# Performance work log

Hardware: AMD Instinct MI355X
Metric: run time of the kernel (lower is better)

The kernel has to match this reference:

```python
import jax, jax.numpy as jnp
import numpy as np

D_MODEL = 1024
NUM_HEADS = 16
D_K = D_MODEL // NUM_HEADS


def setup_inputs() -> dict:
    key = jax.random.key(0)
    ks = jax.random.split(key, 11)
    B, S = 2, 2048
    scale = 1.0 / np.sqrt(D_MODEL)
    inp = {
        "v": jax.random.normal(ks[0], (B, S, D_MODEL), jnp.float32),
        "k": jax.random.normal(ks[1], (B, S, D_MODEL), jnp.float32),
        "q": jax.random.normal(ks[2], (B, S, D_MODEL), jnp.float32),
        "Wv": jax.random.normal(ks[3], (D_MODEL, D_MODEL), jnp.float32) * scale,
        "bv": jax.random.normal(ks[4], (D_MODEL,), jnp.float32) * 0.01,
        "Wk": jax.random.normal(ks[5], (D_MODEL, D_MODEL), jnp.float32) * scale,
        "bk": jax.random.normal(ks[6], (D_MODEL,), jnp.float32) * 0.01,
        "Wq": jax.random.normal(ks[7], (D_MODEL, D_MODEL), jnp.float32) * scale,
        "bq": jax.random.normal(ks[8], (D_MODEL,), jnp.float32) * 0.01,
        "Wo": jax.random.normal(ks[9], (D_MODEL, D_MODEL), jnp.float32) * scale,
        "bo": jax.random.normal(ks[10], (D_MODEL,), jnp.float32) * 0.01,
    }
    return inp


def reference(v, k, q, Wv, bv, Wk, bk, Wq, bq, Wo, bo):
    B, S, _ = q.shape
    # Linear projections (torch Linear: x @ W.T + b)
    vp = v @ Wv.T + bv
    kp = k @ Wk.T + bk
    qp = q @ Wq.T + bq
    # Split heads: [B, S, H, Dk]
    vp = vp.reshape(B, S, NUM_HEADS, D_K)
    kp = kp.reshape(B, S, NUM_HEADS, D_K)
    qp = qp.reshape(B, S, NUM_HEADS, D_K)
    # Scores [B, H, S, S], scaled softmax attention
    scores = jnp.einsum("bqhd,bkhd->bhqk", qp, kp) / jnp.sqrt(jnp.float32(D_K)).astype(qp.dtype)
    attn = jax.nn.softmax(scores, axis=-1)
    out = jnp.einsum("bhqk,bkhd->bqhd", attn, vp)
    out = out.reshape(B, S, D_MODEL)
    return out @ Wo.T + bo
```

## Files before the change

kernel.cpp:

```cpp
#include <hip/hip_runtime.h>
#include <math.h>

#define D 1024
#define NH 16
#define DK 64
#define S_LEN 2048
#define QSCALE 0.18033688011112f

using short8 = __attribute__((ext_vector_type(8))) short;
using f32x4  = __attribute__((ext_vector_type(4))) float;

#define MFMA16(a, b, c) __builtin_amdgcn_mfma_f32_16x16x32_bf16((a), (b), (c), 0, 0, 0)
#define EXP2F(x) __builtin_amdgcn_exp2f(x)

__device__ inline unsigned short f2bf(float f) {
    union { float f; unsigned u; } v; v.f = f;
    unsigned r = v.u + 0x7fffu + ((v.u >> 16) & 1u);
    return (unsigned short)(r >> 16);
}

__device__ inline void gload16(const unsigned short* g, unsigned short* l) {
    __builtin_amdgcn_global_load_lds(
        (const __attribute__((address_space(1))) void*)g,
        (__attribute__((address_space(3))) void*)l, 16, 0, 0);
}

struct CvtP {
    const float* s[7];
    unsigned short* d[7];
};
__global__ __launch_bounds__(256) void cvt_all(CvtP p, int inpBlocks, int wBlocks) {
    int bx = blockIdx.x;
    int seg, boff;
    if (bx < 3 * inpBlocks) { seg = bx / inpBlocks; boff = bx - seg * inpBlocks; }
    else { int t = bx - 3 * inpBlocks; seg = 3 + t / wBlocks; boff = t - (seg - 3) * wBlocks; }
    int i = (boff * 256 + threadIdx.x) * 4;
    float4 f = *(const float4*)(p.s[seg] + i);
    ushort4 u;
    u.x = f2bf(f.x); u.y = f2bf(f.y); u.z = f2bf(f.z); u.w = f2bf(f.w);
    *(ushort4*)(p.d[seg] + i) = u;
}

__global__ __launch_bounds__(256) void gemm_qkv(
    const unsigned short* __restrict__ qb, const unsigned short* __restrict__ kb,
    const unsigned short* __restrict__ vb,
    const unsigned short* __restrict__ Wqb, const unsigned short* __restrict__ Wkb,
    const unsigned short* __restrict__ Wvb,
    const float* __restrict__ bq, const float* __restrict__ bk, const float* __restrict__ bv,
    unsigned short* __restrict__ Qp, unsigned short* __restrict__ Kp,
    unsigned short* __restrict__ Vt)
{
    __shared__ unsigned short sA[128 * 32];
    __shared__ unsigned short sB[64 * 32];

    const int z = blockIdx.z;
    const unsigned short* X = (z == 0) ? qb : (z == 1) ? kb : vb;
    const unsigned short* W = (z == 0) ? Wqb : (z == 1) ? Wkb : Wvb;
    const float* bias = (z == 0) ? bq : (z == 1) ? bk : bv;

    const int tid = threadIdx.x, lane = tid & 63, w = tid >> 6;
    const int wy = w & 1, wx = w >> 1, r = lane & 15, q = lane >> 4;
    const int m0 = blockIdx.x * 128, n0 = blockIdx.y * 64;
    const int lrow = tid >> 2, lkc = (tid & 3) * 8;

    const unsigned short* Xg = X + (size_t)(m0 + lrow) * D + lkc;
    const unsigned short* Wg = W + (size_t)(n0 + lrow) * D + lkc;

    f32x4 acc[4][2];
    #pragma unroll
    for (int mi = 0; mi < 4; ++mi)
        #pragma unroll
        for (int ni = 0; ni < 2; ++ni) acc[mi][ni] = (f32x4){0.f, 0.f, 0.f, 0.f};

    for (int k0 = 0; k0 < D; k0 += 32) {
        __syncthreads();
        gload16(Xg + k0,          sA + w * 512);
        gload16(Xg + 64 * D + k0, sA + 2048 + w * 512);
        gload16(Wg + k0,          sB + w * 512);
        __syncthreads();
        short8 af[4], bfr[2];
        #pragma unroll
        for (int mi = 0; mi < 4; ++mi)
            af[mi] = *(const short8*)(sA + (wy * 64 + mi * 16 + r) * 32 + q * 8);
        #pragma unroll
        for (int ni = 0; ni < 2; ++ni)
            bfr[ni] = *(const short8*)(sB + (wx * 32 + ni * 16 + r) * 32 + q * 8);
        #pragma unroll
        for (int mi = 0; mi < 4; ++mi)
            #pragma unroll
            for (int ni = 0; ni < 2; ++ni)
                acc[mi][ni] = MFMA16(af[mi], bfr[ni], acc[mi][ni]);
    }

    float bcol[2];
    #pragma unroll
    for (int ni = 0; ni < 2; ++ni) bcol[ni] = bias[n0 + wx * 32 + ni * 16 + r];

    #pragma unroll
    for (int mi = 0; mi < 4; ++mi)
        #pragma unroll
        for (int ni = 0; ni < 2; ++ni)
            #pragma unroll
            for (int reg = 0; reg < 4; ++reg) {
                int row = m0 + wy * 64 + mi * 16 + q * 4 + reg;
                int col = n0 + wx * 32 + ni * 16 + r;
                float val = acc[mi][ni][reg] + bcol[ni];
                if (z == 0) {
                    Qp[(size_t)row * D + col] = f2bf(val * QSCALE);
                } else if (z == 1) {
                    Kp[(size_t)row * D + col] = f2bf(val);
                } else {
                    int bb = row >> 11, s = row & (S_LEN - 1);
                    int h = col >> 6, dk = col & 63;
                    Vt[(((size_t)bb * NH + h) * DK + dk) * (size_t)S_LEN + s] = f2bf(val);
                }
            }
}

__global__ __launch_bounds__(256) void gemm_o(
    const unsigned short* __restrict__ X, const unsigned short* __restrict__ W,
    const float* __restrict__ bias, float* __restrict__ out)
{
    __shared__ unsigned short sA[128 * 32];
    __shared__ unsigned short sB[64 * 32];

    const int tid = threadIdx.x, lane = tid & 63, w = tid >> 6;
    const int wy = w & 1, wx = w >> 1, r = lane & 15, q = lane >> 4;
    const int m0 = blockIdx.x * 128, n0 = blockIdx.y * 64;
    const int lrow = tid >> 2, lkc = (tid & 3) * 8;

    const unsigned short* Xg = X + (size_t)(m0 + lrow) * D + lkc;
    const unsigned short* Wg = W + (size_t)(n0 + lrow) * D + lkc;

    f32x4 acc[4][2];
    #pragma unroll
    for (int mi = 0; mi < 4; ++mi)
        #pragma unroll
        for (int ni = 0; ni < 2; ++ni) acc[mi][ni] = (f32x4){0.f, 0.f, 0.f, 0.f};

    for (int k0 = 0; k0 < D; k0 += 32) {
        __syncthreads();
        gload16(Xg + k0,          sA + w * 512);
        gload16(Xg + 64 * D + k0, sA + 2048 + w * 512);
        gload16(Wg + k0,          sB + w * 512);
        __syncthreads();
        short8 af[4], bfr[2];
        #pragma unroll
        for (int mi = 0; mi < 4; ++mi)
            af[mi] = *(const short8*)(sA + (wy * 64 + mi * 16 + r) * 32 + q * 8);
        #pragma unroll
        for (int ni = 0; ni < 2; ++ni)
            bfr[ni] = *(const short8*)(sB + (wx * 32 + ni * 16 + r) * 32 + q * 8);
        #pragma unroll
        for (int mi = 0; mi < 4; ++mi)
            #pragma unroll
            for (int ni = 0; ni < 2; ++ni)
                acc[mi][ni] = MFMA16(af[mi], bfr[ni], acc[mi][ni]);
    }

    float bcol[2];
    #pragma unroll
    for (int ni = 0; ni < 2; ++ni) bcol[ni] = bias[n0 + wx * 32 + ni * 16 + r];

    #pragma unroll
    for (int mi = 0; mi < 4; ++mi)
        #pragma unroll
        for (int ni = 0; ni < 2; ++ni)
            #pragma unroll
            for (int reg = 0; reg < 4; ++reg) {
                int row = m0 + wy * 64 + mi * 16 + q * 4 + reg;
                int col = n0 + wx * 32 + ni * 16 + r;
                out[(size_t)row * D + col] = acc[mi][ni][reg] + bcol[ni];
            }
}

__global__ __launch_bounds__(256) void attn_bf16(
    const unsigned short* __restrict__ Qp, const unsigned short* __restrict__ Kp,
    const unsigned short* __restrict__ Vt, unsigned short* __restrict__ AO)
{
    __shared__ unsigned short sK[2 * 2048];
    __shared__ unsigned short sV[2 * 2048];
    __shared__ unsigned short sP[4][32][72];

    const int tid = threadIdx.x, lane = tid & 63, w = tid >> 6;
    const int r = lane & 15, q = lane >> 4;
    const int q0 = blockIdx.x * 128;
    const int h = blockIdx.y, b = blockIdx.z;
    const int S = S_LEN;

    const unsigned short* Qbase = Qp + ((size_t)b * S + q0 + 32 * w) * D + h * DK;
    short8 qf[2][2];
    #pragma unroll
    for (int rb = 0; rb < 2; ++rb)
        #pragma unroll
        for (int c = 0; c < 2; ++c)
            qf[rb][c] = *(const short8*)(Qbase + (size_t)(rb * 16 + r) * D + c * 32 + q * 8);

    const int srow = tid >> 2, scol = (tid & 3) * 8;
    const unsigned short* Kg = Kp + ((size_t)b * S + srow) * D + h * DK + scol;
    const unsigned short* Vg = Vt + (((size_t)b * NH + h) * DK + srow) * (size_t)S + scol;

    f32x4 O[2][4];
    float psum[2][4];
    #pragma unroll
    for (int rb = 0; rb < 2; ++rb)
        #pragma unroll
        for (int i = 0; i < 4; ++i) { O[rb][i] = (f32x4){0.f, 0.f, 0.f, 0.f}; psum[rb][i] = 0.f; }

    for (int kv0 = 0; kv0 < S; kv0 += 64) {
        __syncthreads();
        gload16(Kg + (size_t)kv0 * D,      sK + w * 512);
        gload16(Kg + (size_t)kv0 * D + 32, sK + 2048 + w * 512);
        gload16(Vg + kv0,                  sV + w * 512);
        gload16(Vg + kv0 + 32,             sV + 2048 + w * 512);
        __syncthreads();

        f32x4 sc[2][4];
        #pragma unroll
        for (int j = 0; j < 4; ++j) {
            short8 kf0 = *(const short8*)(sK + (16 * j + r) * 32 + q * 8);
            short8 kf1 = *(const short8*)(sK + 2048 + (16 * j + r) * 32 + q * 8);
            #pragma unroll
            for (int rb = 0; rb < 2; ++rb) {
                f32x4 t = (f32x4){0.f, 0.f, 0.f, 0.f};
                t = MFMA16(qf[rb][0], kf0, t);
                t = MFMA16(qf[rb][1], kf1, t);
                sc[rb][j] = t;
            }
        }

        #pragma unroll
        for (int rb = 0; rb < 2; ++rb)
            #pragma unroll
            for (int reg = 0; reg < 4; ++reg) {
                float p0 = EXP2F(fminf(sc[rb][0][reg], 30.f));
                float p1 = EXP2F(fminf(sc[rb][1][reg], 30.f));
                float p2 = EXP2F(fminf(sc[rb][2][reg], 30.f));
                float p3 = EXP2F(fminf(sc[rb][3][reg], 30.f));
                psum[rb][reg] += (p0 + p1) + (p2 + p3);
                int row = rb * 16 + q * 4 + reg;
                sP[w][row][r]      = f2bf(p0);
                sP[w][row][16 + r] = f2bf(p1);
                sP[w][row][32 + r] = f2bf(p2);
                sP[w][row][48 + r] = f2bf(p3);
            }

        short8 pf[2][2];
        #pragma unroll
        for (int rb = 0; rb < 2; ++rb) {
            pf[rb][0] = *(const short8*)(&sP[w][rb * 16 + r][q * 8]);
            pf[rb][1] = *(const short8*)(&sP[w][rb * 16 + r][32 + q * 8]);
        }

        #pragma unroll
        for (int nb = 0; nb < 4; ++nb) {
            short8 vf0 = *(const short8*)(sV + (16 * nb + r) * 32 + q * 8);
            short8 vf1 = *(const short8*)(sV + 2048 + (16 * nb + r) * 32 + q * 8);
            #pragma unroll
            for (int rb = 0; rb < 2; ++rb) {
                O[rb][nb] = MFMA16(pf[rb][0], vf0, O[rb][nb]);
                O[rb][nb] = MFMA16(pf[rb][1], vf1, O[rb][nb]);
            }
        }
    }

    float inv[2][4];
    #pragma unroll
    for (int rb = 0; rb < 2; ++rb)
        #pragma unroll
        for (int reg = 0; reg < 4; ++reg) {
            float l = psum[rb][reg];
            #pragma unroll
            for (int off = 8; off > 0; off >>= 1) l += __shfl_xor(l, off);
            inv[rb][reg] = 1.0f / l;
        }

    unsigned short* Ob = AO + ((size_t)b * S + q0 + 32 * w) * D + h * DK;
    #pragma unroll
    for (int rb = 0; rb < 2; ++rb)
        #pragma unroll
        for (int reg = 0; reg < 4; ++reg)
            #pragma unroll
            for (int nb = 0; nb < 4; ++nb)
                Ob[(size_t)(rb * 16 + q * 4 + reg) * D + nb * 16 + r] =
                    f2bf(O[rb][nb][reg] * inv[rb][reg]);
}

extern "C" void kernel_launch(void* const* d_in, const int* in_sizes, int n_in,
                              void* d_out, int out_size, void* d_ws, size_t ws_size,
                              hipStream_t stream)
{
    const float* v  = (const float*)d_in[0];
    const float* k  = (const float*)d_in[1];
    const float* q  = (const float*)d_in[2];
    const float* Wv = (const float*)d_in[3];
    const float* bv = (const float*)d_in[4];
    const float* Wk = (const float*)d_in[5];
    const float* bk = (const float*)d_in[6];
    const float* Wq = (const float*)d_in[7];
    const float* bq = (const float*)d_in[8];
    const float* Wo = (const float*)d_in[9];
    const float* bo = (const float*)d_in[10];
    float* out = (float*)d_out;

    const int BS = in_sizes[0] / D;
    const int S  = S_LEN;
    const int B  = BS / S;

    char* ws = (char*)d_ws;
    unsigned short* qb  = (unsigned short*)(ws);
    unsigned short* kb  = (unsigned short*)(ws + 8388608);
    unsigned short* vb  = (unsigned short*)(ws + 16777216);
    unsigned short* Wqb = (unsigned short*)(ws + 25165824);
    unsigned short* Wkb = (unsigned short*)(ws + 27262976);
    unsigned short* Wvb = (unsigned short*)(ws + 29360128);
    unsigned short* Wob = (unsigned short*)(ws + 31457280);
    unsigned short* Qp  = (unsigned short*)(ws + 33554432);
    unsigned short* Kp  = (unsigned short*)(ws + 41943040);
    unsigned short* Vt  = (unsigned short*)(ws + 50331648);
    unsigned short* AO  = qb;

    dim3 blk(256);
    const int nInp = BS * D, nW = D * D;
    const int inpBlocks = nInp / 1024, wBlocks = nW / 1024;

    CvtP cp;
    cp.s[0] = q;  cp.d[0] = qb;
    cp.s[1] = k;  cp.d[1] = kb;
    cp.s[2] = v;  cp.d[2] = vb;
    cp.s[3] = Wq; cp.d[3] = Wqb;
    cp.s[4] = Wk; cp.d[4] = Wkb;
    cp.s[5] = Wv; cp.d[5] = Wvb;
    cp.s[6] = Wo; cp.d[6] = Wob;
    cvt_all<<<3 * inpBlocks + 4 * wBlocks, blk, 0, stream>>>(cp, inpBlocks, wBlocks);

    dim3 qkvgrid(BS / 128, D / 64, 3);
    gemm_qkv<<<qkvgrid, blk, 0, stream>>>(qb, kb, vb, Wqb, Wkb, Wvb,
                                          bq, bk, bv, Qp, Kp, Vt);

    dim3 agrid(S / 128, NH, B);
    attn_bf16<<<agrid, blk, 0, stream>>>(Qp, Kp, Vt, AO);

    dim3 ogrid(BS / 128, D / 64);
    gemm_o<<<ogrid, blk, 0, stream>>>(AO, Wob, bo, out);
}
```

Measured before the change: 256.5 us.

## Widen QKV GEMM tile to 128x128 and load attention K/V fragments directly from global

```diff
diff --git a/kernel.cpp b/kernel.cpp
--- a/kernel.cpp
+++ b/kernel.cpp
@@ -51,7 +51,7 @@
     unsigned short* __restrict__ Vt)
 {
     __shared__ unsigned short sA[128 * 32];
-    __shared__ unsigned short sB[64 * 32];
+    __shared__ unsigned short sB[128 * 32];
 
     const int z = blockIdx.z;
     const unsigned short* X = (z == 0) ? qb : (z == 1) ? kb : vb;
@@ -60,50 +60,51 @@
 
     const int tid = threadIdx.x, lane = tid & 63, w = tid >> 6;
     const int wy = w & 1, wx = w >> 1, r = lane & 15, q = lane >> 4;
-    const int m0 = blockIdx.x * 128, n0 = blockIdx.y * 64;
+    const int m0 = blockIdx.x * 128, n0 = blockIdx.y * 128;
     const int lrow = tid >> 2, lkc = (tid & 3) * 8;
 
     const unsigned short* Xg = X + (size_t)(m0 + lrow) * D + lkc;
     const unsigned short* Wg = W + (size_t)(n0 + lrow) * D + lkc;
 
-    f32x4 acc[4][2];
+    f32x4 acc[4][4];
     #pragma unroll
     for (int mi = 0; mi < 4; ++mi)
         #pragma unroll
-        for (int ni = 0; ni < 2; ++ni) acc[mi][ni] = (f32x4){0.f, 0.f, 0.f, 0.f};
+        for (int ni = 0; ni < 4; ++ni) acc[mi][ni] = (f32x4){0.f, 0.f, 0.f, 0.f};
 
     for (int k0 = 0; k0 < D; k0 += 32) {
         __syncthreads();
         gload16(Xg + k0,          sA + w * 512);
         gload16(Xg + 64 * D + k0, sA + 2048 + w * 512);
         gload16(Wg + k0,          sB + w * 512);
+        gload16(Wg + 64 * D + k0, sB + 2048 + w * 512);
         __syncthreads();
-        short8 af[4], bfr[2];
+        short8 af[4], bfr[4];
         #pragma unroll
         for (int mi = 0; mi < 4; ++mi)
             af[mi] = *(const short8*)(sA + (wy * 64 + mi * 16 + r) * 32 + q * 8);
         #pragma unroll
-        for (int ni = 0; ni < 2; ++ni)
-            bfr[ni] = *(const short8*)(sB + (wx * 32 + ni * 16 + r) * 32 + q * 8);
+        for (int ni = 0; ni < 4; ++ni)
+            bfr[ni] = *(const short8*)(sB + (wx * 64 + ni * 16 + r) * 32 + q * 8);
         #pragma unroll
         for (int mi = 0; mi < 4; ++mi)
             #pragma unroll
-            for (int ni = 0; ni < 2; ++ni)
+            for (int ni = 0; ni < 4; ++ni)
                 acc[mi][ni] = MFMA16(af[mi], bfr[ni], acc[mi][ni]);
     }
 
-    float bcol[2];
-    #pragma unroll
-    for (int ni = 0; ni < 2; ++ni) bcol[ni] = bias[n0 + wx * 32 + ni * 16 + r];
+    float bcol[4];
+    #pragma unroll
+    for (int ni = 0; ni < 4; ++ni) bcol[ni] = bias[n0 + wx * 64 + ni * 16 + r];
 
     #pragma unroll
     for (int mi = 0; mi < 4; ++mi)
         #pragma unroll
-        for (int ni = 0; ni < 2; ++ni)
+        for (int ni = 0; ni < 4; ++ni)
             #pragma unroll
             for (int reg = 0; reg < 4; ++reg) {
                 int row = m0 + wy * 64 + mi * 16 + q * 4 + reg;
-                int col = n0 + wx * 32 + ni * 16 + r;
+                int col = n0 + wx * 64 + ni * 16 + r;
                 float val = acc[mi][ni][reg] + bcol[ni];
                 if (z == 0) {
                     Qp[(size_t)row * D + col] = f2bf(val * QSCALE);
@@ -174,12 +175,10 @@
             }
 }
 
-__global__ __launch_bounds__(256) void attn_bf16(
+__global__ __launch_bounds__(256, 2) void attn_bf16(
     const unsigned short* __restrict__ Qp, const unsigned short* __restrict__ Kp,
     const unsigned short* __restrict__ Vt, unsigned short* __restrict__ AO)
 {
-    __shared__ unsigned short sK[2 * 2048];
-    __shared__ unsigned short sV[2 * 2048];
     __shared__ unsigned short sP[4][32][72];
 
     const int tid = threadIdx.x, lane = tid & 63, w = tid >> 6;
@@ -196,9 +195,8 @@
         for (int c = 0; c < 2; ++c)
             qf[rb][c] = *(const short8*)(Qbase + (size_t)(rb * 16 + r) * D + c * 32 + q * 8);
 
-    const int srow = tid >> 2, scol = (tid & 3) * 8;
-    const unsigned short* Kg = Kp + ((size_t)b * S + srow) * D + h * DK + scol;
-    const unsigned short* Vg = Vt + (((size_t)b * NH + h) * DK + srow) * (size_t)S + scol;
+    const unsigned short* Kfb = Kp + ((size_t)b * S + r) * D + h * DK + q * 8;
+    const unsigned short* Vfb = Vt + (((size_t)b * NH + h) * DK + r) * (size_t)S + q * 8;
 
     f32x4 O[2][4];
     float psum[2][4];
@@ -208,35 +206,40 @@
         for (int i = 0; i < 4; ++i) { O[rb][i] = (f32x4){0.f, 0.f, 0.f, 0.f}; psum[rb][i] = 0.f; }
 
     for (int kv0 = 0; kv0 < S; kv0 += 64) {
-        __syncthreads();
-        gload16(Kg + (size_t)kv0 * D,      sK + w * 512);
-        gload16(Kg + (size_t)kv0 * D + 32, sK + 2048 + w * 512);
-        gload16(Vg + kv0,                  sV + w * 512);
-        gload16(Vg + kv0 + 32,             sV + 2048 + w * 512);
-        __syncthreads();
+        short8 kf[4][2];
+        #pragma unroll
+        for (int j = 0; j < 4; ++j) {
+            const unsigned short* Krow = Kfb + (size_t)(kv0 + 16 * j) * D;
+            kf[j][0] = *(const short8*)(Krow);
+            kf[j][1] = *(const short8*)(Krow + 32);
+        }
+        short8 vf[4][2];
+        #pragma unroll
+        for (int nb = 0; nb < 4; ++nb) {
+            const unsigned short* Vrow = Vfb + (size_t)(16 * nb) * S + kv0;
+            vf[nb][0] = *(const short8*)(Vrow);
+            vf[nb][1] = *(const short8*)(Vrow + 32);
+        }
 
         f32x4 sc[2][4];
         #pragma unroll
-        for (int j = 0; j < 4; ++j) {
-            short8 kf0 = *(const short8*)(sK + (16 * j + r) * 32 + q * 8);
-            short8 kf1 = *(const short8*)(sK + 2048 + (16 * j + r) * 32 + q * 8);
+        for (int j = 0; j < 4; ++j)
             #pragma unroll
             for (int rb = 0; rb < 2; ++rb) {
                 f32x4 t = (f32x4){0.f, 0.f, 0.f, 0.f};
-                t = MFMA16(qf[rb][0], kf0, t);
-                t = MFMA16(qf[rb][1], kf1, t);
+                t = MFMA16(qf[rb][0], kf[j][0], t);
+                t = MFMA16(qf[rb][1], kf[j][1], t);
                 sc[rb][j] = t;
             }
-        }
 
         #pragma unroll
         for (int rb = 0; rb < 2; ++rb)
             #pragma unroll
             for (int reg = 0; reg < 4; ++reg) {
-                float p0 = EXP2F(fminf(sc[rb][0][reg], 30.f));
-                float p1 = EXP2F(fminf(sc[rb][1][reg], 30.f));
-                float p2 = EXP2F(fminf(sc[rb][2][reg], 30.f));
-                float p3 = EXP2F(fminf(sc[rb][3][reg], 30.f));
+                float p0 = EXP2F(sc[rb][0][reg]);
+                float p1 = EXP2F(sc[rb][1][reg]);
+                float p2 = EXP2F(sc[rb][2][reg]);
+                float p3 = EXP2F(sc[rb][3][reg]);
                 psum[rb][reg] += (p0 + p1) + (p2 + p3);
                 int row = rb * 16 + q * 4 + reg;
                 sP[w][row][r]      = f2bf(p0);
@@ -253,15 +256,12 @@
         }
 
         #pragma unroll
-        for (int nb = 0; nb < 4; ++nb) {
-            short8 vf0 = *(const short8*)(sV + (16 * nb + r) * 32 + q * 8);
-            short8 vf1 = *(const short8*)(sV + 2048 + (16 * nb + r) * 32 + q * 8);
+        for (int nb = 0; nb < 4; ++nb)
             #pragma unroll
             for (int rb = 0; rb < 2; ++rb) {
-                O[rb][nb] = MFMA16(pf[rb][0], vf0, O[rb][nb]);
-                O[rb][nb] = MFMA16(pf[rb][1], vf1, O[rb][nb]);
-            }
-        }
+                O[rb][nb] = MFMA16(pf[rb][0], vf[nb][0], O[rb][nb]);
+                O[rb][nb] = MFMA16(pf[rb][1], vf[nb][1], O[rb][nb]);
+            }
     }
 
     float inv[2][4];
@@ -334,7 +334,7 @@
     cp.s[6] = Wo; cp.d[6] = Wob;
     cvt_all<<<3 * inpBlocks + 4 * wBlocks, blk, 0, stream>>>(cp, inpBlocks, wBlocks);
 
-    dim3 qkvgrid(BS / 128, D / 64, 3);
+    dim3 qkvgrid(BS / 128, D / 128, 3);
     gemm_qkv<<<qkvgrid, blk, 0, stream>>>(qb, kb, vb, Wqb, Wkb, Wvb,
                                           bq, bk, bv, Qp, Kp, Vt);
 
```

New measurement: 311.6 us. 1.22x slower.
